# Kernel optimization log

Hardware: AMD Instinct MI355X
Metric: run time of the kernel (lower is better)

The kernel has to match this reference:

```python
import jax, jax.numpy as jnp
import numpy as np

B = 65536
IN_F = 1024
OUT_F = 1024


def setup_inputs() -> dict:
    key = jax.random.key(0)
    k1, k2 = jax.random.split(key)
    x = jax.random.normal(k1, (B, IN_F), dtype=jnp.float32)
    # init matches torch: normal(0, sqrt(2/(in+out)))
    std = np.sqrt(2.0 / (IN_F + OUT_F)).astype(np.float32)
    weight = jax.random.normal(k2, (OUT_F, IN_F), dtype=jnp.float32) * std
    bias = jnp.zeros((OUT_F,), dtype=jnp.float32)
    return {"x": x, "weight": weight, "bias": bias}


def reference(x, weight, bias):
    # Deterministic binarization: sign(w) in {-1, 0, +1} (sign(0)=0, same as torch)
    w_bin = jnp.sign(weight)
    # [B, in] @ [in, out] + [out]
    return jnp.matmul(x, w_bin.T) + bias[None, :]
```

## Files before the change

kernel.cpp:

```cpp
#include <hip/hip_runtime.h>


typedef __bf16 bf16x8 __attribute__((ext_vector_type(8)));
typedef float  f32x4  __attribute__((ext_vector_type(4)));
typedef int    i32x4  __attribute__((ext_vector_type(4)));
typedef char   i8x16  __attribute__((ext_vector_type(16)));

constexpr int Mdim = 65536, Ndim = 1024, Kdim = 1024;

typedef const __attribute__((address_space(1))) char ga_char;
typedef __attribute__((address_space(3))) char lds_char;
__device__ __forceinline__ void gload16(const void* g, void* l) {
    __builtin_amdgcn_global_load_lds((ga_char*)g, (lds_char*)l, 16, 0, 0);
}
__device__ __forceinline__ f32x4 mfma16(bf16x8 a, bf16x8 b, f32x4 c) {
    return __builtin_amdgcn_mfma_f32_16x16x32_bf16(a, b, c, 0, 0, 0);
}


__global__ __launch_bounds__(256)
void xquant_kernel(const float* __restrict__ X, char* __restrict__ XI,
                   float* __restrict__ SC) {
    const int lane = threadIdx.x & 63;
    const int row  = blockIdx.x * 4 + (threadIdx.x >> 6);
    const float* src = X + (size_t)row * Kdim + lane * 16;
    f32x4 v[4];
#pragma unroll
    for (int k = 0; k < 4; ++k) v[k] = *(const f32x4*)(src + k * 4);
    float m = 0.f;
#pragma unroll
    for (int k = 0; k < 4; ++k)
#pragma unroll
        for (int e = 0; e < 4; ++e) m = fmaxf(m, fabsf(v[k][e]));
#pragma unroll
    for (int i = 1; i < 64; i <<= 1) m = fmaxf(m, __shfl_xor(m, i));
    const float s = (m > 0.f) ? 127.f / m : 0.f;
    i8x16 o;
#pragma unroll
    for (int k = 0; k < 4; ++k)
#pragma unroll
        for (int e = 0; e < 4; ++e)
            o[k * 4 + e] = (char)__float2int_rn(v[k][e] * s);
    const int rowb = row >> 7, mb = (row >> 4) & 7, fr = row & 15;
    const int kt = lane >> 2, hq = lane & 3;
    *(i8x16*)(XI + (size_t)(rowb * 16 + kt) * 8192 + mb * 1024
              + (hq * 16 + fr) * 16) = o;
    if (lane == 0) SC[row] = m * (1.f / 127.f);
}

__global__ __launch_bounds__(256)
void wsign8_kernel(const float* __restrict__ W, char* __restrict__ WI) {
    const int id   = blockIdx.x * 256 + threadIdx.x;
    const int lane = id & 63;
    const int nb   = (id >> 6) & 15;
    const int kt   = (id >> 10) & 15;
    const int colb = id >> 14;
    const float* src = W + (size_t)(colb * 256 + nb * 16 + (lane & 15)) * Kdim
                         + kt * 64 + (lane >> 4) * 16;
    i8x16 o;
#pragma unroll
    for (int k = 0; k < 4; ++k) {
        f32x4 v = *(const f32x4*)(src + k * 4);
#pragma unroll
        for (int e = 0; e < 4; ++e)
            o[k * 4 + e] = (char)((v[e] > 0.f) - (v[e] < 0.f));
    }
    *(i8x16*)(WI + (size_t)id * 16) = o;
}

__global__ __launch_bounds__(512, 4)
void binlin_i8(const char* __restrict__ XI, const char* __restrict__ WI,
               const float* __restrict__ SC, const float* __restrict__ bias,
               float* __restrict__ out)
{
    __shared__ __align__(16) char Al[2][8192];
    __shared__ __align__(16) char Bl[2][16384];

    constexpr int NWG = (Mdim / 128) * (Ndim / 256);
    const int swz  = (blockIdx.x & 7) * (NWG / 8) + (blockIdx.x >> 3);
    const int colb = swz & 3;
    const int rowb = swz >> 2;
    const int row0 = rowb * 128;

    const int tid  = threadIdx.x;
    const int lane = tid & 63;
    const int wid  = tid >> 6;
    const int wr   = wid >> 2;
    const int wcn  = wid & 3;
    const int fr   = lane & 15;
    const int hq   = lane >> 4;

    const char* XIb = XI + (size_t)rowb * 16 * 8192;
    const char* WIb = WI + (size_t)colb * 16 * 16384;

    auto STAGE = [&](int buf, int kt) {
        gload16(XIb + (size_t)kt * 8192 + tid * 16, &Al[buf][tid * 16]);
        const char* bsrc = WIb + (size_t)kt * 16384 + tid * 16;
        gload16(bsrc,        &Bl[buf][tid * 16]);
        gload16(bsrc + 8192, &Bl[buf][8192 + tid * 16]);
    };
    auto lda = [&](int buf, int i) -> i32x4 {
        return *(const i32x4*)(&Al[buf][(wr * 4 + i) * 1024 + lane * 16]);
    };
    auto ldb = [&](int buf, int j) -> i32x4 {
        return *(const i32x4*)(&Bl[buf][(wcn * 4 + j) * 1024 + lane * 16]);
    };

    i32x4 acc[4][4] = {};

    STAGE(0, 0);
    __syncthreads();

    constexpr int NKT = Kdim / 64;
    int cur = 0;
    for (int t = 0; t < NKT; ++t) {
        const int nxt = cur ^ 1;
        const bool pre = (t + 1 < NKT);
        if (pre) STAGE(nxt, t + 1);

        i32x4 af[4];
#pragma unroll
        for (int i = 0; i < 4; ++i) af[i] = lda(cur, i);
        __builtin_amdgcn_s_setprio(1);
#pragma unroll
        for (int j = 0; j < 4; ++j) {
            i32x4 bf = ldb(cur, j);
#pragma unroll
            for (int i = 0; i < 4; ++i)
                acc[i][j] = __builtin_amdgcn_mfma_i32_16x16x64_i8(
                    af[i], bf, acc[i][j], 0, 0, 0);
        }
        __builtin_amdgcn_s_setprio(0);

        if (pre) __syncthreads();
        cur = nxt;
    }

    const int orow = row0 + wr * 64 + hq * 4;
    const int ocol = colb * 256 + wcn * 64 + fr;
    f32x4 sv[4];
#pragma unroll
    for (int i = 0; i < 4; ++i) sv[i] = *(const f32x4*)(SC + orow + i * 16);
#pragma unroll
    for (int j = 0; j < 4; ++j) {
        const float bv = bias[ocol + j * 16];
#pragma unroll
        for (int i = 0; i < 4; ++i)
#pragma unroll
            for (int r = 0; r < 4; ++r)
                out[(size_t)(orow + i * 16 + r) * Ndim + (ocol + j * 16)] =
                    (float)acc[i][j][r] * sv[i][r] + bv;
    }
}


__global__ __launch_bounds__(256)
void wprep_kernel(const float* __restrict__ W, __bf16* __restrict__ WS) {
    const int id   = blockIdx.x * 256 + threadIdx.x;
    const int colb = id >> 15;
    const int kt   = (id >> 10) & 31;
    const int g    = id & 1023;
    const int nb   = g >> 6;
    const int lane = g & 63;
    const int row  = colb * 256 + nb * 16 + (lane & 15);
    const int col  = kt * 32 + (lane >> 4) * 8;
    const float* src = W + (size_t)row * Kdim + col;
    f32x4 a = *(const f32x4*)src;
    f32x4 b = *(const f32x4*)(src + 4);
    bf16x8 o;
#pragma unroll
    for (int e = 0; e < 4; ++e) {
        o[e]     = (__bf16)(float)((a[e] > 0.f) - (a[e] < 0.f));
        o[e + 4] = (__bf16)(float)((b[e] > 0.f) - (b[e] < 0.f));
    }
    *(bf16x8*)(WS + (size_t)id * 8) = o;
}

__global__ __launch_bounds__(512, 4)
void binlin128x256(const float* __restrict__ X, const __bf16* __restrict__ WS,
                   const float* __restrict__ bias, float* __restrict__ out)
{
    __shared__ __align__(16) char Alc[2][128 * 80];
    __shared__ __align__(16) __bf16 Bl[2][256 * 32];
    constexpr int mNWG = (Mdim / 128) * (Ndim / 256);
    const int swz  = (blockIdx.x & 7) * (mNWG / 8) + (blockIdx.x >> 3);
    const int colb = swz & 3;
    const int rowb = swz >> 2;
    const int row0 = rowb * 128;
    const int tid  = threadIdx.x;
    const int lane = tid & 63;
    const int wid  = tid >> 6;
    const int wr   = wid >> 2;
    const int wcn  = wid & 3;
    const int fr   = lane & 15;
    const int hq   = lane >> 4;
    const int a_r  = tid >> 2;
    const int a_c  = (tid & 3) * 8;
    const float* Xb = X + (size_t)(row0 + a_r) * Kdim + a_c;
    const __bf16* WSb = WS + (size_t)colb * 262144;
    f32x4 ra[2];
    auto GLA = [&](int kt) {
        const float* p = Xb + kt * 32;
        ra[0] = *(const f32x4*)p;
        ra[1] = *(const f32x4*)(p + 4);
    };
    auto DSWA = [&](int buf) {
        bf16x8 v;
#pragma unroll
        for (int e = 0; e < 4; ++e) {
            v[e] = (__bf16)ra[0][e]; v[e + 4] = (__bf16)ra[1][e];
        }
        *(bf16x8*)(&Alc[buf][a_r * 80 + a_c * 2]) = v;
    };
    auto GLB = [&](int buf, int kt) {
        const __bf16* s = WSb + (size_t)kt * 8192 + wid * 1024 + lane * 8;
        gload16(s,       &Bl[buf][wid * 1024]);
        gload16(s + 512, &Bl[buf][wid * 1024 + 512]);
    };
    auto lda = [&](int buf, int i) -> bf16x8 {
        const int row = wr * 64 + i * 16 + fr;
        return *(const bf16x8*)(&Alc[buf][row * 80 + hq * 16]);
    };
    auto ldb = [&](int buf, int j) -> bf16x8 {
        return *(const bf16x8*)(&Bl[buf][(wcn * 4 + j) * 512 + lane * 8]);
    };
    f32x4 acc[4][4] = {};
    GLA(0); GLB(0, 0); DSWA(0);
    __syncthreads();
    int cur = 0;
    for (int t = 0; t < 32; ++t) {
        const int nxt = cur ^ 1;
        const bool pre = (t + 1 < 32);
        if (pre) { GLA(t + 1); GLB(nxt, t + 1); }
        bf16x8 af[4];
#pragma unroll
        for (int i = 0; i < 4; ++i) af[i] = lda(cur, i);
        __builtin_amdgcn_s_setprio(1);
#pragma unroll
        for (int j = 0; j < 4; ++j) {
            bf16x8 bfr = ldb(cur, j);
#pragma unroll
            for (int i = 0; i < 4; ++i)
                acc[i][j] = mfma16(af[i], bfr, acc[i][j]);
        }
        __builtin_amdgcn_s_setprio(0);
        if (pre) { DSWA(nxt); __syncthreads(); }
        cur = nxt;
    }
    const int orow = row0 + wr * 64 + hq * 4;
    const int ocol = colb * 256 + wcn * 64 + fr;
#pragma unroll
    for (int j = 0; j < 4; ++j) {
        const float bv = bias[ocol + j * 16];
#pragma unroll
        for (int i = 0; i < 4; ++i)
#pragma unroll
            for (int r = 0; r < 4; ++r)
                out[(size_t)(orow + i * 16 + r) * Ndim + (ocol + j * 16)] =
                    acc[i][j][r] + bv;
    }
}

__global__ __launch_bounds__(256)
void binlin_fallback(const float* __restrict__ X, const float* __restrict__ Wf,
                     const float* __restrict__ bias, float* __restrict__ out)
{
    __shared__ __align__(16) __bf16 Al[2][128][32];
    __shared__ __align__(16) __bf16 Bl[2][128][32];
    const int swz  = (blockIdx.x & 7) * (4096 / 8) + (blockIdx.x >> 3);
    const int colb = swz & 7, rowb = swz >> 3;
    const int row0 = rowb * 128, col0 = colb * 128;
    const int tid = threadIdx.x, lane = tid & 63, wid = tid >> 6;
    const int wr = wid >> 1, wc = wid & 1;
    const int sr = tid >> 2, sc = (tid & 3) * 8;
    const float* Xb = X + (size_t)row0 * Kdim;
    const float* Wb = Wf + (size_t)col0 * Kdim;
    f32x4 ra[2][2], rb[2][2];
    auto GL = [&](int k0) {
#pragma unroll
        for (int p = 0; p < 2; ++p) {
            const float* sa = Xb + (size_t)(p * 64 + sr) * Kdim + k0 + sc;
            ra[p][0] = *(const f32x4*)sa; ra[p][1] = *(const f32x4*)(sa + 4);
            const float* sb = Wb + (size_t)(p * 64 + sr) * Kdim + k0 + sc;
            rb[p][0] = *(const f32x4*)sb; rb[p][1] = *(const f32x4*)(sb + 4);
        }
    };
    auto DSW = [&](int buf) {
#pragma unroll
        for (int p = 0; p < 2; ++p) {
            bf16x8 va, vb;
#pragma unroll
            for (int e = 0; e < 4; ++e) {
                va[e] = (__bf16)ra[p][0][e]; va[e + 4] = (__bf16)ra[p][1][e];
                float a = rb[p][0][e], b = rb[p][1][e];
                vb[e] = (__bf16)(float)((a > 0.f) - (a < 0.f));
                vb[e + 4] = (__bf16)(float)((b > 0.f) - (b < 0.f));
            }
            *(bf16x8*)&Al[buf][p * 64 + sr][sc] = va;
            *(bf16x8*)&Bl[buf][p * 64 + sr][sc] = vb;
        }
    };
    f32x4 acc[4][4] = {};
    const int fr = lane & 15, ks = (lane >> 4) * 8;
    auto COMP = [&](int buf) {
        bf16x8 af[4], bf[4];
#pragma unroll
        for (int i = 0; i < 4; ++i) af[i] = *(const bf16x8*)&Al[buf][wr * 64 + fr + i * 16][ks];
#pragma unroll
        for (int j = 0; j < 4; ++j) bf[j] = *(const bf16x8*)&Bl[buf][wc * 64 + fr + j * 16][ks];
#pragma unroll
        for (int i = 0; i < 4; ++i)
#pragma unroll
            for (int j = 0; j < 4; ++j)
                acc[i][j] = mfma16(af[i], bf[j], acc[i][j]);
    };
    GL(0); DSW(0); __syncthreads();
    int cur = 0;
    for (int t = 0; t < 32; ++t) {
        if (t + 1 < 32) GL((t + 1) * 32);
        COMP(cur);
        if (t + 1 < 32) { DSW(cur ^ 1); __syncthreads(); cur ^= 1; }
    }
    const int orow = row0 + wr * 64 + (lane >> 4) * 4;
    const int ocol = col0 + wc * 64 + fr;
#pragma unroll
    for (int j = 0; j < 4; ++j) {
        const float bv = bias[ocol + j * 16];
#pragma unroll
        for (int i = 0; i < 4; ++i)
#pragma unroll
            for (int r = 0; r < 4; ++r)
                out[(size_t)(orow + i * 16 + r) * Ndim + (ocol + j * 16)] = acc[i][j][r] + bv;
    }
}

extern "C" void kernel_launch(void* const* d_in, const int* in_sizes, int n_in,
                              void* d_out, int out_size, void* d_ws, size_t ws_size,
                              hipStream_t stream) {
    const float* x  = (const float*)d_in[0];
    const float* w  = (const float*)d_in[1];
    const float* b  = (const float*)d_in[2];
    float* out      = (float*)d_out;

    constexpr size_t WI_BYTES = (size_t)Ndim * Kdim;
    constexpr size_t SC_BYTES = (size_t)Mdim * sizeof(float);
    constexpr size_t XI_BYTES = (size_t)Mdim * Kdim;
    constexpr size_t I8_TOTAL = WI_BYTES + SC_BYTES + XI_BYTES;
    constexpr size_t WS_BYTES = (size_t)Ndim * Kdim * sizeof(__bf16);

    if (ws_size >= I8_TOTAL) {
        char*  wi = (char*)d_ws;
        float* sc = (float*)((char*)d_ws + WI_BYTES);
        char*  xi = (char*)d_ws + WI_BYTES + SC_BYTES;
        wsign8_kernel<<<dim3(256),   dim3(256), 0, stream>>>(w, wi);
        xquant_kernel<<<dim3(16384), dim3(256), 0, stream>>>(x, xi, sc);
        binlin_i8<<<dim3(2048), dim3(512), 0, stream>>>(xi, wi, sc, b, out);
    } else if (ws_size >= WS_BYTES) {
        __bf16* ws = (__bf16*)d_ws;
        wprep_kernel<<<dim3(512), dim3(256), 0, stream>>>(w, ws);
        binlin128x256<<<dim3(2048), dim3(512), 0, stream>>>(x, ws, b, out);
    } else {
        binlin_fallback<<<dim3(4096), dim3(256), 0, stream>>>(x, w, b, out);
    }
}
```

Measured before the change: 220.5 us.

## Load int8 GEMM fragments directly from global into registers, dropping LDS staging

```diff
diff --git a/kernel.cpp b/kernel.cpp
--- a/kernel.cpp
+++ b/kernel.cpp
@@ -15,6 +15,9 @@
 }
 __device__ __forceinline__ f32x4 mfma16(bf16x8 a, bf16x8 b, f32x4 c) {
     return __builtin_amdgcn_mfma_f32_16x16x32_bf16(a, b, c, 0, 0, 0);
+}
+__device__ __forceinline__ i32x4 mfma_i8(i32x4 a, i32x4 b, i32x4 c) {
+    return __builtin_amdgcn_mfma_i32_16x16x64_i8(a, b, c, 0, 0, 0);
 }
 
 
@@ -68,14 +71,11 @@
     *(i8x16*)(WI + (size_t)id * 16) = o;
 }
 
-__global__ __launch_bounds__(512, 4)
-void binlin_i8(const char* __restrict__ XI, const char* __restrict__ WI,
-               const float* __restrict__ SC, const float* __restrict__ bias,
-               float* __restrict__ out)
+__global__ __launch_bounds__(512)
+void binlin_i8nl(const char* __restrict__ XI, const char* __restrict__ WI,
+                 const float* __restrict__ SC, const float* __restrict__ bias,
+                 float* __restrict__ out)
 {
-    __shared__ __align__(16) char Al[2][8192];
-    __shared__ __align__(16) char Bl[2][16384];
-
     constexpr int NWG = (Mdim / 128) * (Ndim / 256);
     const int swz  = (blockIdx.x & 7) * (NWG / 8) + (blockIdx.x >> 3);
     const int colb = swz & 3;
@@ -90,51 +90,39 @@
     const int fr   = lane & 15;
     const int hq   = lane >> 4;
 
-    const char* XIb = XI + (size_t)rowb * 16 * 8192;
-    const char* WIb = WI + (size_t)colb * 16 * 16384;
-
-    auto STAGE = [&](int buf, int kt) {
-        gload16(XIb + (size_t)kt * 8192 + tid * 16, &Al[buf][tid * 16]);
-        const char* bsrc = WIb + (size_t)kt * 16384 + tid * 16;
-        gload16(bsrc,        &Bl[buf][tid * 16]);
-        gload16(bsrc + 8192, &Bl[buf][8192 + tid * 16]);
-    };
-    auto lda = [&](int buf, int i) -> i32x4 {
-        return *(const i32x4*)(&Al[buf][(wr * 4 + i) * 1024 + lane * 16]);
-    };
-    auto ldb = [&](int buf, int j) -> i32x4 {
-        return *(const i32x4*)(&Bl[buf][(wcn * 4 + j) * 1024 + lane * 16]);
-    };
+    const char* Ab = XI + (size_t)rowb * 16 * 8192 + (wr * 4) * 1024 + lane * 16;
+    const char* Bb = WI + (size_t)colb * 16 * 16384 + (wcn * 4) * 1024 + lane * 16;
 
     i32x4 acc[4][4] = {};
-
-    STAGE(0, 0);
-    __syncthreads();
+    i32x4 a0[4], b0[4], a1[4], b1[4];
+
+#define LOADSET(As, Bs, kt) do {                                              \
+    _Pragma("unroll")                                                         \
+    for (int i = 0; i < 4; ++i)                                               \
+        As[i] = *(const i32x4*)(Ab + (size_t)(kt) * 8192 + i * 1024);         \
+    _Pragma("unroll")                                                         \
+    for (int j = 0; j < 4; ++j)                                               \
+        Bs[j] = *(const i32x4*)(Bb + (size_t)(kt) * 16384 + j * 1024);        \
+} while (0)
+
+#define MFMASET(As, Bs) do {                                                  \
+    _Pragma("unroll")                                                         \
+    for (int j = 0; j < 4; ++j)                                               \
+        _Pragma("unroll")                                                     \
+        for (int i = 0; i < 4; ++i)                                           \
+            acc[i][j] = mfma_i8(As[i], Bs[j], acc[i][j]);                     \
+} while (0)
 
     constexpr int NKT = Kdim / 64;
-    int cur = 0;
-    for (int t = 0; t < NKT; ++t) {
-        const int nxt = cur ^ 1;
-        const bool pre = (t + 1 < NKT);
-        if (pre) STAGE(nxt, t + 1);
-
-        i32x4 af[4];
-#pragma unroll
-        for (int i = 0; i < 4; ++i) af[i] = lda(cur, i);
-        __builtin_amdgcn_s_setprio(1);
-#pragma unroll
-        for (int j = 0; j < 4; ++j) {
-            i32x4 bf = ldb(cur, j);
-#pragma unroll
-            for (int i = 0; i < 4; ++i)
-                acc[i][j] = __builtin_amdgcn_mfma_i32_16x16x64_i8(
-                    af[i], bf, acc[i][j], 0, 0, 0);
-        }
-        __builtin_amdgcn_s_setprio(0);
-
-        if (pre) __syncthreads();
-        cur = nxt;
-    }
+    LOADSET(a0, b0, 0);
+    for (int t = 0; t < NKT; t += 2) {
+        LOADSET(a1, b1, t + 1);
+        MFMASET(a0, b0);
+        if (t + 2 < NKT) LOADSET(a0, b0, t + 2);
+        MFMASET(a1, b1);
+    }
+#undef LOADSET
+#undef MFMASET
 
     const int orow = row0 + wr * 64 + hq * 4;
     const int ocol = colb * 256 + wcn * 64 + fr;
@@ -354,7 +342,7 @@
         char*  xi = (char*)d_ws + WI_BYTES + SC_BYTES;
         wsign8_kernel<<<dim3(256),   dim3(256), 0, stream>>>(w, wi);
         xquant_kernel<<<dim3(16384), dim3(256), 0, stream>>>(x, xi, sc);
-        binlin_i8<<<dim3(2048), dim3(512), 0, stream>>>(xi, wi, sc, b, out);
+        binlin_i8nl<<<dim3(2048), dim3(512), 0, stream>>>(xi, wi, sc, b, out);
     } else if (ws_size >= WS_BYTES) {
         __bf16* ws = (__bf16*)d_ws;
         wprep_kernel<<<dim3(512), dim3(256), 0, stream>>>(w, ws);
```

After: 289.6 us. +31.4%, slower.

## Switch int8 GEMM to 32x32x32 MFMA with matching operand layouts

Applied to the files above, without the earlier changes.

```diff
diff --git a/kernel.cpp b/kernel.cpp
--- a/kernel.cpp
+++ b/kernel.cpp
@@ -4,6 +4,7 @@
 typedef __bf16 bf16x8 __attribute__((ext_vector_type(8)));
 typedef float  f32x4  __attribute__((ext_vector_type(4)));
 typedef int    i32x4  __attribute__((ext_vector_type(4)));
+typedef int    i32x16 __attribute__((ext_vector_type(16)));
 typedef char   i8x16  __attribute__((ext_vector_type(16)));
 
 constexpr int Mdim = 65536, Ndim = 1024, Kdim = 1024;
@@ -19,11 +20,11 @@
 
 
 __global__ __launch_bounds__(256)
-void xquant_kernel(const float* __restrict__ X, char* __restrict__ XI,
-                   float* __restrict__ SC) {
-    const int lane = threadIdx.x & 63;
-    const int row  = blockIdx.x * 4 + (threadIdx.x >> 6);
-    const float* src = X + (size_t)row * Kdim + lane * 16;
+void xquant32_kernel(const float* __restrict__ X, char* __restrict__ XI,
+                     float* __restrict__ SC) {
+    const int l   = threadIdx.x & 63;
+    const int row = blockIdx.x * 4 + (threadIdx.x >> 6);
+    const float* src = X + (size_t)row * Kdim + l * 16;
     f32x4 v[4];
 #pragma unroll
     for (int k = 0; k < 4; ++k) v[k] = *(const f32x4*)(src + k * 4);
@@ -41,22 +42,18 @@
 #pragma unroll
         for (int e = 0; e < 4; ++e)
             o[k * 4 + e] = (char)__float2int_rn(v[k][e] * s);
-    const int rowb = row >> 7, mb = (row >> 4) & 7, fr = row & 15;
-    const int kt = lane >> 2, hq = lane & 3;
-    *(i8x16*)(XI + (size_t)(rowb * 16 + kt) * 8192 + mb * 1024
-              + (hq * 16 + fr) * 16) = o;
-    if (lane == 0) SC[row] = m * (1.f / 127.f);
+    const size_t tile = (size_t)(row >> 7) * 16 + (l >> 2);
+    const int u  = (((row >> 5) & 3) << 1) | ((l >> 1) & 1);
+    const int L  = ((l & 1) << 5) | (row & 31);
+    *(i8x16*)(XI + tile * 8192 + u * 1024 + L * 16) = o;
+    if (l == 0) SC[row] = m * (1.f / 127.f);
 }
 
 __global__ __launch_bounds__(256)
-void wsign8_kernel(const float* __restrict__ W, char* __restrict__ WI) {
-    const int id   = blockIdx.x * 256 + threadIdx.x;
-    const int lane = id & 63;
-    const int nb   = (id >> 6) & 15;
-    const int kt   = (id >> 10) & 15;
-    const int colb = id >> 14;
-    const float* src = W + (size_t)(colb * 256 + nb * 16 + (lane & 15)) * Kdim
-                         + kt * 64 + (lane >> 4) * 16;
+void wsign32_kernel(const float* __restrict__ W, char* __restrict__ WI) {
+    const int l = threadIdx.x & 63;
+    const int n = blockIdx.x * 4 + (threadIdx.x >> 6);
+    const float* src = W + (size_t)n * Kdim + l * 16;
     i8x16 o;
 #pragma unroll
     for (int k = 0; k < 4; ++k) {
@@ -65,13 +62,16 @@
         for (int e = 0; e < 4; ++e)
             o[k * 4 + e] = (char)((v[e] > 0.f) - (v[e] < 0.f));
     }
-    *(i8x16*)(WI + (size_t)id * 16) = o;
+    const size_t tile = (size_t)(n >> 8) * 16 + (l >> 2);
+    const int u  = (((n >> 5) & 7) << 1) | ((l >> 1) & 1);
+    const int L  = ((l & 1) << 5) | (n & 31);
+    *(i8x16*)(WI + tile * 16384 + u * 1024 + L * 16) = o;
 }
 
 __global__ __launch_bounds__(512, 4)
-void binlin_i8(const char* __restrict__ XI, const char* __restrict__ WI,
-               const float* __restrict__ SC, const float* __restrict__ bias,
-               float* __restrict__ out)
+void binlin_i8w32(const char* __restrict__ XI, const char* __restrict__ WI,
+                  const float* __restrict__ SC, const float* __restrict__ bias,
+                  float* __restrict__ out)
 {
     __shared__ __align__(16) char Al[2][8192];
     __shared__ __align__(16) char Bl[2][16384];
@@ -80,15 +80,14 @@
     const int swz  = (blockIdx.x & 7) * (NWG / 8) + (blockIdx.x >> 3);
     const int colb = swz & 3;
     const int rowb = swz >> 2;
-    const int row0 = rowb * 128;
 
     const int tid  = threadIdx.x;
     const int lane = tid & 63;
     const int wid  = tid >> 6;
     const int wr   = wid >> 2;
     const int wcn  = wid & 3;
-    const int fr   = lane & 15;
-    const int hq   = lane >> 4;
+    const int l31  = lane & 31;
+    const int h    = lane >> 5;
 
     const char* XIb = XI + (size_t)rowb * 16 * 8192;
     const char* WIb = WI + (size_t)colb * 16 * 16384;
@@ -99,14 +98,14 @@
         gload16(bsrc,        &Bl[buf][tid * 16]);
         gload16(bsrc + 8192, &Bl[buf][8192 + tid * 16]);
     };
-    auto lda = [&](int buf, int i) -> i32x4 {
-        return *(const i32x4*)(&Al[buf][(wr * 4 + i) * 1024 + lane * 16]);
-    };
-    auto ldb = [&](int buf, int j) -> i32x4 {
-        return *(const i32x4*)(&Bl[buf][(wcn * 4 + j) * 1024 + lane * 16]);
-    };
-
-    i32x4 acc[4][4] = {};
+    auto lda = [&](int buf, int ii, int kb) -> i32x4 {
+        return *(const i32x4*)(&Al[buf][(((wr * 2 + ii) << 1) | kb) * 1024 + lane * 16]);
+    };
+    auto ldb = [&](int buf, int jj, int kb) -> i32x4 {
+        return *(const i32x4*)(&Bl[buf][(((wcn * 2 + jj) << 1) | kb) * 1024 + lane * 16]);
+    };
+
+    i32x16 acc[2][2] = {};
 
     STAGE(0, 0);
     __syncthreads();
@@ -118,38 +117,46 @@
         const bool pre = (t + 1 < NKT);
         if (pre) STAGE(nxt, t + 1);
 
-        i32x4 af[4];
-#pragma unroll
-        for (int i = 0; i < 4; ++i) af[i] = lda(cur, i);
+        i32x4 a[2][2], b[2][2];
+#pragma unroll
+        for (int kb = 0; kb < 2; ++kb)
+#pragma unroll
+            for (int q = 0; q < 2; ++q) {
+                a[kb][q] = lda(cur, q, kb);
+                b[kb][q] = ldb(cur, q, kb);
+            }
         __builtin_amdgcn_s_setprio(1);
 #pragma unroll
-        for (int j = 0; j < 4; ++j) {
-            i32x4 bf = ldb(cur, j);
-#pragma unroll
-            for (int i = 0; i < 4; ++i)
-                acc[i][j] = __builtin_amdgcn_mfma_i32_16x16x64_i8(
-                    af[i], bf, acc[i][j], 0, 0, 0);
-        }
+        for (int kb = 0; kb < 2; ++kb)
+#pragma unroll
+            for (int ii = 0; ii < 2; ++ii)
+#pragma unroll
+                for (int jj = 0; jj < 2; ++jj)
+                    acc[ii][jj] = __builtin_amdgcn_mfma_i32_32x32x32_i8(
+                        a[kb][ii], b[kb][jj], acc[ii][jj], 0, 0, 0);
         __builtin_amdgcn_s_setprio(0);
 
         if (pre) __syncthreads();
         cur = nxt;
     }
 
-    const int orow = row0 + wr * 64 + hq * 4;
-    const int ocol = colb * 256 + wcn * 64 + fr;
-    f32x4 sv[4];
-#pragma unroll
-    for (int i = 0; i < 4; ++i) sv[i] = *(const f32x4*)(SC + orow + i * 16);
-#pragma unroll
-    for (int j = 0; j < 4; ++j) {
-        const float bv = bias[ocol + j * 16];
-#pragma unroll
-        for (int i = 0; i < 4; ++i)
-#pragma unroll
-            for (int r = 0; r < 4; ++r)
-                out[(size_t)(orow + i * 16 + r) * Ndim + (ocol + j * 16)] =
-                    (float)acc[i][j][r] * sv[i][r] + bv;
+#pragma unroll
+    for (int ii = 0; ii < 2; ++ii) {
+        const int orow = rowb * 128 + wr * 64 + ii * 32 + h * 4;
+        f32x4 sv[4];
+#pragma unroll
+        for (int q = 0; q < 4; ++q) sv[q] = *(const f32x4*)(SC + orow + q * 8);
+#pragma unroll
+        for (int jj = 0; jj < 2; ++jj) {
+            const int ocol = colb * 256 + wcn * 64 + jj * 32 + l31;
+            const float bv = bias[ocol];
+#pragma unroll
+            for (int q = 0; q < 4; ++q)
+#pragma unroll
+                for (int e = 0; e < 4; ++e)
+                    out[(size_t)(orow + q * 8 + e) * Ndim + ocol] =
+                        (float)acc[ii][jj][q * 4 + e] * sv[q][e] + bv;
+        }
     }
 }
 
@@ -352,9 +359,9 @@
         char*  wi = (char*)d_ws;
         float* sc = (float*)((char*)d_ws + WI_BYTES);
         char*  xi = (char*)d_ws + WI_BYTES + SC_BYTES;
-        wsign8_kernel<<<dim3(256),   dim3(256), 0, stream>>>(w, wi);
-        xquant_kernel<<<dim3(16384), dim3(256), 0, stream>>>(x, xi, sc);
-        binlin_i8<<<dim3(2048), dim3(512), 0, stream>>>(xi, wi, sc, b, out);
+        wsign32_kernel<<<dim3(256),   dim3(256), 0, stream>>>(w, wi);
+        xquant32_kernel<<<dim3(16384), dim3(256), 0, stream>>>(x, xi, sc);
+        binlin_i8w32<<<dim3(2048), dim3(512), 0, stream>>>(xi, wi, sc, b, out);
     } else if (ws_size >= WS_BYTES) {
         __bf16* ws = (__bf16*)d_ws;
         wprep_kernel<<<dim3(512), dim3(256), 0, stream>>>(w, ws);
```

Result: no change. 223.2 us (+1.2%).
